# Performance work log

Measured on AMD Instinct MI355X. Metric: run time of the kernel, lower is better.

## Reference

```python
import jax
import jax.numpy as jnp
from jax import lax
import numpy as np

# module hyperparameters (match init_kwargs)
IN_C, OUT_C = 32, 64
K, STRIDE, PAD, DIL = 3, 1, 1, 1
GRID_SIZE, ORDER = 5, 3
GRID_LO, GRID_HI = -1.0, 1.0
SCALE_SPLINE = 1.0
EPS = 1e-8


def _knot_grid():
    # grid = arange(-order, grid_size+order+1) * h + lo ; length = grid_size + 2*order + 1 = 12
    h = (GRID_HI - GRID_LO) / GRID_SIZE
    return jnp.arange(-ORDER, GRID_SIZE + ORDER + 1, dtype=jnp.float32) * h + GRID_LO


def _bspline_bases(x):
    """Cox-de Boor recursion. x: (N, P) -> bases: (N, P, GRID_SIZE+ORDER)."""
    grid = _knot_grid()
    xe = x[..., None]  # (N, P, 1)
    bases = ((xe >= grid[:-1]) & (xe < grid[1:])).astype(x.dtype)  # (N, P, 11)
    for k in range(1, ORDER + 1):
        left_den = jnp.maximum(grid[k:-1] - grid[:-(k + 1)], EPS)
        right_den = jnp.maximum(grid[k + 1:] - grid[1:-k], EPS)
        bases = ((xe - grid[:-(k + 1)]) / left_den * bases[..., :-1]
                 + (grid[k + 1:] - xe) / right_den * bases[..., 1:])
    return bases  # (N, P, 8)


def setup_inputs() -> dict:
    key = jax.random.key(0)
    k1, k2, k3 = jax.random.split(key, 3)
    x = jax.random.normal(k1, (4, IN_C, 56, 56), dtype=jnp.float32)
    base_weight = jax.random.normal(k2, (OUT_C, IN_C, K, K), dtype=jnp.float32) * 0.05
    spline_weight = jax.random.normal(k3, (OUT_C, IN_C * K * K, GRID_SIZE + ORDER), dtype=jnp.float32) * 0.05
    spline_scaler = jnp.ones((OUT_C,), dtype=jnp.float32)
    return {"x": x, "base_weight": base_weight,
            "spline_weight": spline_weight, "spline_scaler": spline_scaler}


def reference(x, base_weight, spline_weight, spline_scaler):
    B, C, H, W = x.shape
    pad = [(PAD, PAD), (PAD, PAD)]
    # base path: conv2d -> SiLU
    base_conv = lax.conv_general_dilated(
        x, base_weight, window_strides=(STRIDE, STRIDE), padding=pad,
        rhs_dilation=(DIL, DIL), dimension_numbers=("NCHW", "OIHW", "NCHW"))
    base_out = jax.nn.silu(base_conv)

    # unfold: (B, C*K*K, oh, ow) with torch Unfold channel ordering (c, kh, kw)
    patches = lax.conv_general_dilated_patches(
        x, filter_shape=(K, K), window_strides=(STRIDE, STRIDE), padding=pad,
        rhs_dilation=(DIL, DIL))
    oh, ow = patches.shape[2], patches.shape[3]
    num_patches = oh * ow
    # (B*num_patches, C*K*K)
    pf = patches.reshape(B, C * K * K, num_patches).transpose(0, 2, 1).reshape(-1, C * K * K)

    bases = _bspline_bases(pf)  # (N, P, F)
    # contract patch-dim and basis-dim against spline weights
    spl = jnp.einsum("npf,opf->no", bases, spline_weight) * spline_scaler  # (N, O)
    spl = spl.reshape(B, num_patches, OUT_C).transpose(0, 2, 1).reshape(B, OUT_C, oh, ow)
    return base_out + SCALE_SPLINE * spl
```

## Files before the change

kernel.cpp:

```cpp
#include <hip/hip_runtime.h>
#include <math.h>


typedef __attribute__((ext_vector_type(8)))  short bf16x8;
typedef __attribute__((ext_vector_type(4)))  float f32x4;
typedef __attribute__((ext_vector_type(16))) float f32x16;

#define MFMA32(a, b, c) __builtin_amdgcn_mfma_f32_32x32x16_bf16((a), (b), (c), 0, 0, 0)

__device__ __forceinline__ unsigned short f2bf(float f) {
    unsigned u = __builtin_bit_cast(unsigned, f);
    u = (u + 0x7fffu + ((u >> 16) & 1u)) >> 16;
    return (unsigned short)u;
}

__device__ __forceinline__ void eval_bases(float v, float bs[8]) {
    #pragma unroll
    for (int i = 0; i < 8; ++i) bs[i] = 0.0f;
    float t = (v + 2.2f) * 2.5f;
    if (t >= 0.0f && t < 11.0f) {
        int j = (int)t;
        if (j > 10) j = 10;
        float knot = (float)(j - 3) * 0.4f - 1.0f;
        float u  = (v - knot) * 2.5f;
        float um = 1.0f - u;
        float u2 = u * u, u3 = u2 * u;
        const float s6 = 1.0f / 6.0f;
        float w0 = um * um * um * s6;
        float w1 = (3.0f * u3 - 6.0f * u2 + 4.0f) * s6;
        float w2 = (-3.0f * u3 + 3.0f * u2 + 3.0f * u + 1.0f) * s6;
        float w3 = u3 * s6;
        int i0 = j - 3;
        if (i0 >= 0)               bs[i0]     = w0;
        if (i0 + 1 >= 0 && i0 < 7) bs[i0 + 1] = w1;
        if (i0 + 2 >= 0 && i0 < 6) bs[i0 + 2] = w2;
        if (i0 + 3 <= 7)           bs[i0 + 3] = w3;
    }
}

__global__ __launch_bounds__(256)
void cvt_swz_kernel(const float* __restrict__ ws, const float* __restrict__ wb,
                    unsigned short* __restrict__ wst, unsigned short* __restrict__ wbt) {
    int i = blockIdx.x * 256 + threadIdx.x;
    if (i < 147456) {
        int j = i & 7, l = (i >> 3) & 63, t = i >> 9;
        int s = t % 144, nf = t / 144;
        int oc = nf * 32 + (l & 31);
        int k  = s * 16 + (l >> 5) * 8 + j;
        wst[i] = f2bf(ws[oc * 2304 + k]);
    } else {
        int i2 = i - 147456;
        if (i2 < 18432) {
            int j = i2 & 7, l = (i2 >> 3) & 63, t = i2 >> 9;
            int s = t % 18, nf = t / 18;
            int oc = nf * 32 + (l & 31);
            int k  = s * 16 + (l >> 5) * 8 + j;
            wbt[i2] = f2bf(wb[oc * 288 + k]);
        }
    }
}

__global__ __launch_bounds__(256)
void kan_mfma_kernel(const float* __restrict__ x,
                     const float* __restrict__ sc,
                     const unsigned short* __restrict__ wst,
                     const unsigned short* __restrict__ wbt,
                     float* __restrict__ out) {
    __shared__ unsigned short smem[26752];
    unsigned short* sb    = smem;
    unsigned short* sx    = smem + 15360;
    unsigned short* patch = smem + 17280;

    const int tid = threadIdx.x;
    const int bx  = blockIdx.x;
    const int b   = bx / 98;
    const int r   = bx - b * 98;
    const int ty  = r / 7;
    const int tx  = r - ty * 7;
    const int h0  = ty * 4, w0 = tx * 8;

    for (int i = tid; i < 1920; i += 256) {
        int c  = i / 60;
        int hp = i - c * 60;
        int hy = hp / 10;
        int hx = hp - hy * 10;
        int hh = h0 + hy - 1, ww = w0 + hx - 1;
        float v = 0.0f;
        if ((unsigned)hh < 56u && (unsigned)ww < 56u)
            v = x[((b * 32 + c) * 56 + hh) * 56 + ww];
        float bs[8];
        eval_bases(v, bs);
        bf16x8 pk;
        #pragma unroll
        for (int j2 = 0; j2 < 8; ++j2) pk[j2] = (short)f2bf(bs[j2]);
        *reinterpret_cast<bf16x8*>(&sb[i * 8]) = pk;
        sx[i] = f2bf(v);
    }
    __syncthreads();

    {
        int m2 = tid >> 3;
        int c0 = (tid & 7) * 4;
        const unsigned short* rsx = &sx[c0 * 60 + (m2 >> 3) * 10 + (m2 & 7)];
        unsigned short* wp = &patch[m2 * 296 + c0 * 9];
        #pragma unroll
        for (int cc = 0; cc < 4; ++cc)
            #pragma unroll
            for (int kh = 0; kh < 3; ++kh)
                #pragma unroll
                for (int kw = 0; kw < 3; ++kw)
                    wp[cc * 9 + kh * 3 + kw] = rsx[cc * 60 + kh * 10 + kw];
    }
    __syncthreads();

    const int lane = tid & 63;
    const int wv   = tid >> 6;
    const int nf   = wv & 1;
    const int kh2  = wv >> 1;
    const int m    = lane & 31;
    const int kg   = lane >> 5;
    const int py0  = m >> 3, px0 = m & 7;

    f32x16 accS = {0.f}; f32x16 accB = {0.f};
    #pragma unroll
    for (int i = 0; i < 16; ++i) { accS[i] = 0.f; accB[i] = 0.f; }

    int aoff[9];
    #pragma unroll
    for (int u = 0; u < 9; ++u) {
        int t2  = 2 * u + kg;
        int dc  = t2 / 9;
        int tap = t2 - dc * 9;
        int kh  = tap / 3;
        int kw  = tap - kh * 3;
        aoff[u] = (dc * 60 + (py0 + kh) * 10 + (px0 + kw)) * 8;
    }

    const unsigned short* bp = wst + ((nf * 144 + kh2 * 72) * 64 + lane) * 8;
    int cbase = kh2 * 7680;
    for (int g = 0; g < 8; ++g) {
        #pragma unroll
        for (int u = 0; u < 9; ++u) {
            bf16x8 a = *reinterpret_cast<const bf16x8*>(&sb[cbase + aoff[u]]);
            bf16x8 bw = *reinterpret_cast<const bf16x8*>(bp + (g * 9 + u) * 512);
            accS = MFMA32(a, bw, accS);
        }
        cbase += 960;
    }

    {
        const unsigned short* ap  = &patch[m * 296 + kg * 8];
        const unsigned short* bbp = wbt + ((nf * 18 + kh2 * 9) * 64 + lane) * 8;
        #pragma unroll
        for (int s = 0; s < 9; ++s) {
            bf16x8 a = *reinterpret_cast<const bf16x8*>(ap + (kh2 * 9 + s) * 16);
            bf16x8 bw = *reinterpret_cast<const bf16x8*>(bbp + s * 512);
            accB = MFMA32(a, bw, accB);
        }
    }

    __syncthreads();
    float* red = (float*)smem;
    if (kh2 == 1) {
        float* dst = red + (nf * 64 + lane) * 36;
        #pragma unroll
        for (int rq = 0; rq < 4; ++rq) {
            f32x4 vS, vB;
            #pragma unroll
            for (int rr = 0; rr < 4; ++rr) { vS[rr] = accS[rq*4+rr]; vB[rr] = accB[rq*4+rr]; }
            *reinterpret_cast<f32x4*>(dst + rq * 4)      = vS;
            *reinterpret_cast<f32x4*>(dst + 16 + rq * 4) = vB;
        }
    }
    __syncthreads();

    if (kh2 == 0) {
        const float* src = red + (nf * 64 + lane) * 36;
        #pragma unroll
        for (int rq = 0; rq < 4; ++rq) {
            f32x4 vS = *reinterpret_cast<const f32x4*>(src + rq * 4);
            f32x4 vB = *reinterpret_cast<const f32x4*>(src + 16 + rq * 4);
            #pragma unroll
            for (int rr = 0; rr < 4; ++rr) { accS[rq*4+rr] += vS[rr]; accB[rq*4+rr] += vB[rr]; }
        }
        const int col = lane & 31;
        const int oc  = nf * 32 + col;
        const float scv = sc[oc];
        const int kg5 = lane >> 5;
        float* ob = out + ((b * 64 + oc) * 56 + h0) * 56 + w0 + 4 * kg5;
        #pragma unroll
        for (int rq = 0; rq < 4; ++rq) {
            f32x4 res;
            #pragma unroll
            for (int rr = 0; rr < 4; ++rr) {
                float bv = accB[rq * 4 + rr];
                float si = bv / (1.0f + __expf(-bv));
                res[rr] = si + scv * accS[rq * 4 + rr];
            }
            *reinterpret_cast<f32x4*>(ob + rq * 56) = res;
        }
    }
}

extern "C" void kernel_launch(void* const* d_in, const int* in_sizes, int n_in,
                              void* d_out, int out_size, void* d_ws, size_t ws_size,
                              hipStream_t stream) {
    const float* x  = (const float*)d_in[0];
    const float* wb = (const float*)d_in[1];
    const float* ws = (const float*)d_in[2];
    const float* sc = (const float*)d_in[3];
    float* out = (float*)d_out;

    unsigned short* wst = (unsigned short*)d_ws;
    unsigned short* wbt = wst + 147456;

    cvt_swz_kernel<<<648, 256, 0, stream>>>(ws, wb, wst, wbt);
    kan_mfma_kernel<<<392, 256, 0, stream>>>(x, sc, wst, wbt, out);
}
```

Baseline: 78.46 us.

## Prefetch weight fragments in registers and scatter im2col directly from staging

The fused MFMA kernel now double-buffers B-weight fragments in registers, so global loads for the next group are issued before the current group's MFMAs. It also splits the spline accumulation across two accumulators to shorten the dependency chain. The first weight fragments are loaded before the x tile is read. The patch matrix is scattered straight from the loaded values, which removes the intermediate sx buffer and one barrier. The cost is much higher register pressure (bufA/bufB plus three accumulators) under a launch_bounds occupancy hint of 3, which risks spills.

```diff
diff --git a/kernel.cpp b/kernel.cpp
--- a/kernel.cpp
+++ b/kernel.cpp
@@ -60,16 +60,15 @@
     }
 }
 
-__global__ __launch_bounds__(256)
+__global__ __launch_bounds__(256, 3)
 void kan_mfma_kernel(const float* __restrict__ x,
                      const float* __restrict__ sc,
                      const unsigned short* __restrict__ wst,
                      const unsigned short* __restrict__ wbt,
                      float* __restrict__ out) {
-    __shared__ unsigned short smem[26752];
+    __shared__ unsigned short smem[24832];
     unsigned short* sb    = smem;
-    unsigned short* sx    = smem + 15360;
-    unsigned short* patch = smem + 17280;
+    unsigned short* patch = smem + 15360;
 
     const int tid = threadIdx.x;
     const int bx  = blockIdx.x;
@@ -79,40 +78,6 @@
     const int tx  = r - ty * 7;
     const int h0  = ty * 4, w0 = tx * 8;
 
-    for (int i = tid; i < 1920; i += 256) {
-        int c  = i / 60;
-        int hp = i - c * 60;
-        int hy = hp / 10;
-        int hx = hp - hy * 10;
-        int hh = h0 + hy - 1, ww = w0 + hx - 1;
-        float v = 0.0f;
-        if ((unsigned)hh < 56u && (unsigned)ww < 56u)
-            v = x[((b * 32 + c) * 56 + hh) * 56 + ww];
-        float bs[8];
-        eval_bases(v, bs);
-        bf16x8 pk;
-        #pragma unroll
-        for (int j2 = 0; j2 < 8; ++j2) pk[j2] = (short)f2bf(bs[j2]);
-        *reinterpret_cast<bf16x8*>(&sb[i * 8]) = pk;
-        sx[i] = f2bf(v);
-    }
-    __syncthreads();
-
-    {
-        int m2 = tid >> 3;
-        int c0 = (tid & 7) * 4;
-        const unsigned short* rsx = &sx[c0 * 60 + (m2 >> 3) * 10 + (m2 & 7)];
-        unsigned short* wp = &patch[m2 * 296 + c0 * 9];
-        #pragma unroll
-        for (int cc = 0; cc < 4; ++cc)
-            #pragma unroll
-            for (int kh = 0; kh < 3; ++kh)
-                #pragma unroll
-                for (int kw = 0; kw < 3; ++kw)
-                    wp[cc * 9 + kh * 3 + kw] = rsx[cc * 60 + kh * 10 + kw];
-    }
-    __syncthreads();
-
     const int lane = tid & 63;
     const int wv   = tid >> 6;
     const int nf   = wv & 1;
@@ -121,9 +86,8 @@
     const int kg   = lane >> 5;
     const int py0  = m >> 3, px0 = m & 7;
 
-    f32x16 accS = {0.f}; f32x16 accB = {0.f};
-    #pragma unroll
-    for (int i = 0; i < 16; ++i) { accS[i] = 0.f; accB[i] = 0.f; }
+    const unsigned short* bp  = wst + ((nf * 144 + kh2 * 72) * 64 + lane) * 8;
+    const unsigned short* bbp = wbt + ((nf * 18  + kh2 * 9 ) * 64 + lane) * 8;
 
     int aoff[9];
     #pragma unroll
@@ -136,28 +100,102 @@
         aoff[u] = (dc * 60 + (py0 + kh) * 10 + (px0 + kw)) * 8;
     }
 
-    const unsigned short* bp = wst + ((nf * 144 + kh2 * 72) * 64 + lane) * 8;
+    bf16x8 bufA[9], bufB[9];
+    #pragma unroll
+    for (int u = 0; u < 9; ++u)
+        bufA[u] = *reinterpret_cast<const bf16x8*>(bp + u * 512);
+
+    float vv[8];
+    #pragma unroll
+    for (int j = 0; j < 8; ++j) {
+        int i = tid + j * 256;
+        float val = 0.0f;
+        if (i < 1920) {
+            int c  = i / 60;
+            int hp = i - c * 60;
+            int hy = hp / 10;
+            int hx = hp - hy * 10;
+            int hh = h0 + hy - 1, ww = w0 + hx - 1;
+            if ((unsigned)hh < 56u && (unsigned)ww < 56u)
+                val = x[((b * 32 + c) * 56 + hh) * 56 + ww];
+        }
+        vv[j] = val;
+    }
+    #pragma unroll
+    for (int j = 0; j < 8; ++j) {
+        int i = tid + j * 256;
+        if (i < 1920) {
+            int c  = i / 60;
+            int hp = i - c * 60;
+            int hy = hp / 10;
+            int hx = hp - hy * 10;
+            float bs[8];
+            eval_bases(vv[j], bs);
+            bf16x8 pk;
+            #pragma unroll
+            for (int j2 = 0; j2 < 8; ++j2) pk[j2] = (short)f2bf(bs[j2]);
+            *reinterpret_cast<bf16x8*>(&sb[i * 8]) = pk;
+            unsigned short xb = f2bf(vv[j]);
+            #pragma unroll
+            for (int kh = 0; kh < 3; ++kh) {
+                int py = hy - kh;
+                if ((unsigned)py < 4u) {
+                    #pragma unroll
+                    for (int kw = 0; kw < 3; ++kw) {
+                        int px = hx - kw;
+                        if ((unsigned)px < 8u)
+                            patch[(py * 8 + px) * 296 + c * 9 + kh * 3 + kw] = xb;
+                    }
+                }
+            }
+        }
+    }
+    __syncthreads();
+
+    f32x16 acc0, acc1, accB;
+    #pragma unroll
+    for (int i = 0; i < 16; ++i) { acc0[i] = 0.f; acc1[i] = 0.f; accB[i] = 0.f; }
+
     int cbase = kh2 * 7680;
-    for (int g = 0; g < 8; ++g) {
+    for (int g = 0; g < 8; g += 2) {
+        #pragma unroll
+        for (int u = 0; u < 9; ++u)
+            bufB[u] = *reinterpret_cast<const bf16x8*>(bp + ((g + 1) * 9 + u) * 512);
         #pragma unroll
         for (int u = 0; u < 9; ++u) {
             bf16x8 a = *reinterpret_cast<const bf16x8*>(&sb[cbase + aoff[u]]);
-            bf16x8 bw = *reinterpret_cast<const bf16x8*>(bp + (g * 9 + u) * 512);
-            accS = MFMA32(a, bw, accS);
+            if (u & 1) acc1 = MFMA32(a, bufA[u], acc1);
+            else       acc0 = MFMA32(a, bufA[u], acc0);
         }
         cbase += 960;
+        if (g + 2 < 8) {
+            #pragma unroll
+            for (int u = 0; u < 9; ++u)
+                bufA[u] = *reinterpret_cast<const bf16x8*>(bp + ((g + 2) * 9 + u) * 512);
+        }
+        #pragma unroll
+        for (int u = 0; u < 9; ++u) {
+            bf16x8 a = *reinterpret_cast<const bf16x8*>(&sb[cbase + aoff[u]]);
+            if (u & 1) acc1 = MFMA32(a, bufB[u], acc1);
+            else       acc0 = MFMA32(a, bufB[u], acc0);
+        }
+        cbase += 960;
     }
 
     {
-        const unsigned short* ap  = &patch[m * 296 + kg * 8];
-        const unsigned short* bbp = wbt + ((nf * 18 + kh2 * 9) * 64 + lane) * 8;
+        #pragma unroll
+        for (int s = 0; s < 9; ++s)
+            bufA[s] = *reinterpret_cast<const bf16x8*>(bbp + s * 512);
+        const unsigned short* ap = &patch[m * 296 + kh2 * 144 + kg * 8];
         #pragma unroll
         for (int s = 0; s < 9; ++s) {
-            bf16x8 a = *reinterpret_cast<const bf16x8*>(ap + (kh2 * 9 + s) * 16);
-            bf16x8 bw = *reinterpret_cast<const bf16x8*>(bbp + s * 512);
-            accB = MFMA32(a, bw, accB);
-        }
-    }
+            bf16x8 a = *reinterpret_cast<const bf16x8*>(ap + s * 16);
+            accB = MFMA32(a, bufA[s], accB);
+        }
+    }
+
+    #pragma unroll
+    for (int i = 0; i < 16; ++i) acc0[i] += acc1[i];
 
     __syncthreads();
     float* red = (float*)smem;
@@ -167,7 +205,7 @@
         for (int rq = 0; rq < 4; ++rq) {
             f32x4 vS, vB;
             #pragma unroll
-            for (int rr = 0; rr < 4; ++rr) { vS[rr] = accS[rq*4+rr]; vB[rr] = accB[rq*4+rr]; }
+            for (int rr = 0; rr < 4; ++rr) { vS[rr] = acc0[rq*4+rr]; vB[rr] = accB[rq*4+rr]; }
             *reinterpret_cast<f32x4*>(dst + rq * 4)      = vS;
             *reinterpret_cast<f32x4*>(dst + 16 + rq * 4) = vB;
         }
@@ -181,13 +219,12 @@
             f32x4 vS = *reinterpret_cast<const f32x4*>(src + rq * 4);
             f32x4 vB = *reinterpret_cast<const f32x4*>(src + 16 + rq * 4);
             #pragma unroll
-            for (int rr = 0; rr < 4; ++rr) { accS[rq*4+rr] += vS[rr]; accB[rq*4+rr] += vB[rr]; }
+            for (int rr = 0; rr < 4; ++rr) { acc0[rq*4+rr] += vS[rr]; accB[rq*4+rr] += vB[rr]; }
         }
         const int col = lane & 31;
         const int oc  = nf * 32 + col;
         const float scv = sc[oc];
-        const int kg5 = lane >> 5;
-        float* ob = out + ((b * 64 + oc) * 56 + h0) * 56 + w0 + 4 * kg5;
+        float* ob = out + ((b * 64 + oc) * 56 + h0) * 56 + w0 + 4 * kg;
         #pragma unroll
         for (int rq = 0; rq < 4; ++rq) {
             f32x4 res;
@@ -195,7 +232,7 @@
             for (int rr = 0; rr < 4; ++rr) {
                 float bv = accB[rq * 4 + rr];
                 float si = bv / (1.0f + __expf(-bv));
-                res[rr] = si + scv * accS[rq * 4 + rr];
+                res[rr] = si + scv * acc0[rq * 4 + rr];
             }
             *reinterpret_cast<f32x4*>(ob + rq * 56) = res;
         }
```

Result: no change. 78.40 us (-0.1%).

## Switch to 16x16 MFMA tiles with 8 waves and drop split-K reduction

Applied to the files above, without the earlier changes.

Replaces the 32x32x16 MFMA scheme (4 waves, K split across two wave pairs and then reduced through shared memory) with 16x16x32 MFMA tiles spread over 8 waves, each owning a 16x16 output tile with the full K range. This removes the cross-wave reduction and its extra barriers. It also builds the im2col patch buffer directly from registers in the same pass as the basis evaluation, which drops the staging array and one sync, and it batches the global loads ahead of the compute. In exchange each wave now streams the full weight K range, so weight traffic per wave grows, and the patch writes are scattered.

```diff
diff --git a/kernel.cpp b/kernel.cpp
--- a/kernel.cpp
+++ b/kernel.cpp
@@ -2,11 +2,10 @@
 #include <math.h>
 
 
-typedef __attribute__((ext_vector_type(8)))  short bf16x8;
-typedef __attribute__((ext_vector_type(4)))  float f32x4;
-typedef __attribute__((ext_vector_type(16))) float f32x16;
-
-#define MFMA32(a, b, c) __builtin_amdgcn_mfma_f32_32x32x16_bf16((a), (b), (c), 0, 0, 0)
+typedef __attribute__((ext_vector_type(8))) short bf16x8;
+typedef __attribute__((ext_vector_type(4))) float f32x4;
+
+#define MFMA16(a, b, c) __builtin_amdgcn_mfma_f32_16x16x32_bf16((a), (b), (c), 0, 0, 0)
 
 __device__ __forceinline__ unsigned short f2bf(float f) {
     unsigned u = __builtin_bit_cast(unsigned, f);
@@ -44,32 +43,31 @@
     int i = blockIdx.x * 256 + threadIdx.x;
     if (i < 147456) {
         int j = i & 7, l = (i >> 3) & 63, t = i >> 9;
-        int s = t % 144, nf = t / 144;
-        int oc = nf * 32 + (l & 31);
-        int k  = s * 16 + (l >> 5) * 8 + j;
+        int S = t % 72, nq = t / 72;
+        int oc = nq * 16 + (l & 15);
+        int k  = S * 32 + (l >> 4) * 8 + j;
         wst[i] = f2bf(ws[oc * 2304 + k]);
     } else {
         int i2 = i - 147456;
         if (i2 < 18432) {
             int j = i2 & 7, l = (i2 >> 3) & 63, t = i2 >> 9;
-            int s = t % 18, nf = t / 18;
-            int oc = nf * 32 + (l & 31);
-            int k  = s * 16 + (l >> 5) * 8 + j;
+            int s = t % 9, nq = t / 9;
+            int oc = nq * 16 + (l & 15);
+            int k  = s * 32 + (l >> 4) * 8 + j;
             wbt[i2] = f2bf(wb[oc * 288 + k]);
         }
     }
 }
 
-__global__ __launch_bounds__(256)
+__global__ __launch_bounds__(512)
 void kan_mfma_kernel(const float* __restrict__ x,
                      const float* __restrict__ sc,
                      const unsigned short* __restrict__ wst,
                      const unsigned short* __restrict__ wbt,
                      float* __restrict__ out) {
-    __shared__ unsigned short smem[26752];
+    __shared__ unsigned short smem[24832];
     unsigned short* sb    = smem;
-    unsigned short* sx    = smem + 15360;
-    unsigned short* patch = smem + 17280;
+    unsigned short* patch = smem + 15360;
 
     const int tid = threadIdx.x;
     const int bx  = blockIdx.x;
@@ -79,127 +77,113 @@
     const int tx  = r - ty * 7;
     const int h0  = ty * 4, w0 = tx * 8;
 
-    for (int i = tid; i < 1920; i += 256) {
-        int c  = i / 60;
-        int hp = i - c * 60;
-        int hy = hp / 10;
-        int hx = hp - hy * 10;
-        int hh = h0 + hy - 1, ww = w0 + hx - 1;
-        float v = 0.0f;
-        if ((unsigned)hh < 56u && (unsigned)ww < 56u)
-            v = x[((b * 32 + c) * 56 + hh) * 56 + ww];
-        float bs[8];
-        eval_bases(v, bs);
-        bf16x8 pk;
-        #pragma unroll
-        for (int j2 = 0; j2 < 8; ++j2) pk[j2] = (short)f2bf(bs[j2]);
-        *reinterpret_cast<bf16x8*>(&sb[i * 8]) = pk;
-        sx[i] = f2bf(v);
-    }
-    __syncthreads();
-
-    {
-        int m2 = tid >> 3;
-        int c0 = (tid & 7) * 4;
-        const unsigned short* rsx = &sx[c0 * 60 + (m2 >> 3) * 10 + (m2 & 7)];
-        unsigned short* wp = &patch[m2 * 296 + c0 * 9];
-        #pragma unroll
-        for (int cc = 0; cc < 4; ++cc)
-            #pragma unroll
-            for (int kh = 0; kh < 3; ++kh)
-                #pragma unroll
-                for (int kw = 0; kw < 3; ++kw)
-                    wp[cc * 9 + kh * 3 + kw] = rsx[cc * 60 + kh * 10 + kw];
-    }
-    __syncthreads();
-
     const int lane = tid & 63;
     const int wv   = tid >> 6;
-    const int nf   = wv & 1;
-    const int kh2  = wv >> 1;
-    const int m    = lane & 31;
-    const int kg   = lane >> 5;
+    const int nq   = wv & 3;
+    const int mh   = wv >> 2;
+    const int ml   = lane & 15;
+    const int kg   = lane >> 4;
+    const int m    = mh * 16 + ml;
     const int py0  = m >> 3, px0 = m & 7;
 
-    f32x16 accS = {0.f}; f32x16 accB = {0.f};
-    #pragma unroll
-    for (int i = 0; i < 16; ++i) { accS[i] = 0.f; accB[i] = 0.f; }
+    float vv[4];
+    #pragma unroll
+    for (int j = 0; j < 4; ++j) {
+        int i = tid + j * 512;
+        float val = 0.0f;
+        if (i < 1920) {
+            int c  = i / 60;
+            int hp = i - c * 60;
+            int hy = hp / 10;
+            int hx = hp - hy * 10;
+            int hh = h0 + hy - 1, ww = w0 + hx - 1;
+            if ((unsigned)hh < 56u && (unsigned)ww < 56u)
+                val = x[((b * 32 + c) * 56 + hh) * 56 + ww];
+        }
+        vv[j] = val;
+    }
+    #pragma unroll
+    for (int j = 0; j < 4; ++j) {
+        int i = tid + j * 512;
+        if (i < 1920) {
+            int c  = i / 60;
+            int hp = i - c * 60;
+            int hy = hp / 10;
+            int hx = hp - hy * 10;
+            float bs[8];
+            eval_bases(vv[j], bs);
+            bf16x8 pk;
+            #pragma unroll
+            for (int j2 = 0; j2 < 8; ++j2) pk[j2] = (short)f2bf(bs[j2]);
+            *reinterpret_cast<bf16x8*>(&sb[i * 8]) = pk;
+            unsigned short xb = f2bf(vv[j]);
+            #pragma unroll
+            for (int kh = 0; kh < 3; ++kh) {
+                int py = hy - kh;
+                if ((unsigned)py < 4u) {
+                    #pragma unroll
+                    for (int kw = 0; kw < 3; ++kw) {
+                        int px = hx - kw;
+                        if ((unsigned)px < 8u)
+                            patch[(py * 8 + px) * 296 + c * 9 + kh * 3 + kw] = xb;
+                    }
+                }
+            }
+        }
+    }
+    __syncthreads();
 
     int aoff[9];
     #pragma unroll
     for (int u = 0; u < 9; ++u) {
-        int t2  = 2 * u + kg;
-        int dc  = t2 / 9;
-        int tap = t2 - dc * 9;
+        int tt  = 4 * u + kg;
+        int dc  = tt / 9;
+        int tap = tt - dc * 9;
         int kh  = tap / 3;
         int kw  = tap - kh * 3;
         aoff[u] = (dc * 60 + (py0 + kh) * 10 + (px0 + kw)) * 8;
     }
 
-    const unsigned short* bp = wst + ((nf * 144 + kh2 * 72) * 64 + lane) * 8;
-    int cbase = kh2 * 7680;
+    f32x4 accS = {0.f, 0.f, 0.f, 0.f};
+    f32x4 accB = {0.f, 0.f, 0.f, 0.f};
+
+    const unsigned short* bp = wst + (nq * 72 * 64 + lane) * 8;
+    int cbase = 0;
     for (int g = 0; g < 8; ++g) {
         #pragma unroll
         for (int u = 0; u < 9; ++u) {
-            bf16x8 a = *reinterpret_cast<const bf16x8*>(&sb[cbase + aoff[u]]);
+            bf16x8 a  = *reinterpret_cast<const bf16x8*>(&sb[cbase + aoff[u]]);
             bf16x8 bw = *reinterpret_cast<const bf16x8*>(bp + (g * 9 + u) * 512);
-            accS = MFMA32(a, bw, accS);
-        }
-        cbase += 960;
+            accS = MFMA16(a, bw, accS);
+        }
+        cbase += 1920;
     }
 
     {
-        const unsigned short* ap  = &patch[m * 296 + kg * 8];
-        const unsigned short* bbp = wbt + ((nf * 18 + kh2 * 9) * 64 + lane) * 8;
+        const unsigned short* ap  = patch + m * 296 + kg * 8;
+        const unsigned short* bbp = wbt + (nq * 9 * 64 + lane) * 8;
         #pragma unroll
         for (int s = 0; s < 9; ++s) {
-            bf16x8 a = *reinterpret_cast<const bf16x8*>(ap + (kh2 * 9 + s) * 16);
+            bf16x8 a  = *reinterpret_cast<const bf16x8*>(ap + s * 32);
             bf16x8 bw = *reinterpret_cast<const bf16x8*>(bbp + s * 512);
-            accB = MFMA32(a, bw, accB);
-        }
-    }
-
-    __syncthreads();
-    float* red = (float*)smem;
-    if (kh2 == 1) {
-        float* dst = red + (nf * 64 + lane) * 36;
-        #pragma unroll
-        for (int rq = 0; rq < 4; ++rq) {
-            f32x4 vS, vB;
-            #pragma unroll
-            for (int rr = 0; rr < 4; ++rr) { vS[rr] = accS[rq*4+rr]; vB[rr] = accB[rq*4+rr]; }
-            *reinterpret_cast<f32x4*>(dst + rq * 4)      = vS;
-            *reinterpret_cast<f32x4*>(dst + 16 + rq * 4) = vB;
-        }
-    }
-    __syncthreads();
-
-    if (kh2 == 0) {
-        const float* src = red + (nf * 64 + lane) * 36;
-        #pragma unroll
-        for (int rq = 0; rq < 4; ++rq) {
-            f32x4 vS = *reinterpret_cast<const f32x4*>(src + rq * 4);
-            f32x4 vB = *reinterpret_cast<const f32x4*>(src + 16 + rq * 4);
-            #pragma unroll
-            for (int rr = 0; rr < 4; ++rr) { accS[rq*4+rr] += vS[rr]; accB[rq*4+rr] += vB[rr]; }
-        }
-        const int col = lane & 31;
-        const int oc  = nf * 32 + col;
-        const float scv = sc[oc];
-        const int kg5 = lane >> 5;
-        float* ob = out + ((b * 64 + oc) * 56 + h0) * 56 + w0 + 4 * kg5;
-        #pragma unroll
-        for (int rq = 0; rq < 4; ++rq) {
-            f32x4 res;
-            #pragma unroll
-            for (int rr = 0; rr < 4; ++rr) {
-                float bv = accB[rq * 4 + rr];
-                float si = bv / (1.0f + __expf(-bv));
-                res[rr] = si + scv * accS[rq * 4 + rr];
-            }
-            *reinterpret_cast<f32x4*>(ob + rq * 56) = res;
-        }
-    }
+            accB = MFMA16(a, bw, accB);
+        }
+    }
+
+    const int oc  = nq * 16 + ml;
+    const float scv = sc[oc];
+    const int rowb = mh * 16 + kg * 4;
+    const int py   = rowb >> 3;
+    const int pxb  = rowb & 7;
+    float* ob = out + ((b * 64 + oc) * 56 + h0 + py) * 56 + w0 + pxb;
+    f32x4 res;
+    #pragma unroll
+    for (int reg = 0; reg < 4; ++reg) {
+        float bv = accB[reg];
+        float si = bv / (1.0f + __expf(-bv));
+        res[reg] = si + scv * accS[reg];
+    }
+    *reinterpret_cast<f32x4*>(ob) = res;
 }
 
 extern "C" void kernel_launch(void* const* d_in, const int* in_sizes, int n_in,
@@ -215,5 +199,5 @@
     unsigned short* wbt = wst + 147456;
 
     cvt_swz_kernel<<<648, 256, 0, stream>>>(ws, wb, wst, wbt);
-    kan_mfma_kernel<<<392, 256, 0, stream>>>(x, sc, wst, wbt, out);
-}
+    kan_mfma_kernel<<<392, 512, 0, stream>>>(x, sc, wst, wbt, out);
+}
```

Measured after the change: 78.27 us (median of 2 runs). Within noise of the previous version (-0.2%).
